# Kernel optimization log

Measured on AMD Instinct MI355X. Metric: run time of the kernel, lower is better.

Reference implementation:

```python
import jax, jax.numpy as jnp
import numpy as np

IN_FEATURES = 100000
OUT_FEATURES = 256

def setup_inputs() -> dict:
    key = jax.random.key(0)
    k1, k2 = jax.random.split(key)
    size = IN_FEATURES
    # adj: COO indices [2, nnz] with nnz == size (values are all ones in the module)
    adj = jax.random.randint(k1, (2, size), 0, size, dtype=jnp.int64)
    weight = jax.random.normal(k2, (IN_FEATURES, OUT_FEATURES), dtype=jnp.float32) * (1.0 / np.sqrt(IN_FEATURES))
    return {"adj": adj, "size": size, "weight": weight}

def reference(adj, size, weight):
    # sparse (size, size) COO with values=1 at (adj[0], adj[1]), times dense weight:
    # out[r] = sum over edges (r, c) of 1.0 * weight[c]
    rows = adj[0]
    cols = adj[1]
    gathered = weight[cols]  # [nnz, out_features] gather
    out = jax.ops.segment_sum(gathered, rows, num_segments=size)  # [size, out_features]
    return out
```

## Files before the change

### kernel.cpp

```cpp
#include <hip/hip_runtime.h>


constexpr int OUT_F = 256;
constexpr int CAP = 8;
constexpr int MAXOVF = 16384;

using f32x4 = __attribute__((ext_vector_type(4))) float;
using i32x4 = __attribute__((ext_vector_type(4))) int;


__global__ __launch_bounds__(256) void fill_k(const int* __restrict__ rows,
                                              const int* __restrict__ cols,
                                              int* __restrict__ counts,
                                              int* __restrict__ bucket,
                                              int* __restrict__ ovf_n,
                                              int* __restrict__ ovf,
                                              int nnz) {
    int e = blockIdx.x * 256 + threadIdx.x;
    if (e >= nnz) return;
    int r = rows[e];
    int c = cols[e];
    int slot = atomicAdd(&counts[r], 1);
    if (slot < CAP) {
        bucket[r * CAP + slot] = c;
    } else {
        int o = atomicAdd(ovf_n, 1);
        if (o < MAXOVF) { ovf[2 * o] = r; ovf[2 * o + 1] = c; }
    }
}


__device__ __forceinline__ void ovf_scan(f32x4& acc, int row,
                                         const int* __restrict__ ovf_n,
                                         const int* __restrict__ ovf,
                                         const f32x4* __restrict__ w4, int lane) {
    int m = *ovf_n; if (m > MAXOVF) m = MAXOVF;
    for (int j = 0; j < m; j++) {
        if (ovf[2 * j] == row)
            acc += w4[(size_t)ovf[2 * j + 1] * 64 + lane];
    }
}

__device__ __forceinline__ void rare_tail(f32x4& acc, int n, const i32x4& b0,
                                          const i32x4* __restrict__ bucket4, int row,
                                          const f32x4* __restrict__ w4, int lane,
                                          const int* __restrict__ ovf_n,
                                          const int* __restrict__ ovf) {
    int m = n < CAP ? n : CAP;
    acc += w4[(size_t)__builtin_amdgcn_readfirstlane(b0.z) * 64 + lane];
    if (m > 3) acc += w4[(size_t)__builtin_amdgcn_readfirstlane(b0.w) * 64 + lane];
    if (m > 4) {
        i32x4 b1 = __builtin_nontemporal_load(bucket4 + (size_t)row * 2 + 1);
        acc += w4[(size_t)__builtin_amdgcn_readfirstlane(b1.x) * 64 + lane];
        if (m > 5) acc += w4[(size_t)__builtin_amdgcn_readfirstlane(b1.y) * 64 + lane];
        if (m > 6) acc += w4[(size_t)__builtin_amdgcn_readfirstlane(b1.z) * 64 + lane];
        if (m > 7) acc += w4[(size_t)__builtin_amdgcn_readfirstlane(b1.w) * 64 + lane];
        if (n > CAP) ovf_scan(acc, row, ovf_n, ovf, w4, lane);
    }
}

__global__ __launch_bounds__(256) void gather_k(const int* __restrict__ counts,
                                                const i32x4* __restrict__ bucket4,
                                                const f32x4* __restrict__ w4,
                                                f32x4* __restrict__ out4,
                                                const int* __restrict__ ovf_n,
                                                const int* __restrict__ ovf,
                                                int nrows) {
    const int lane = threadIdx.x & 63;
    int wid = (blockIdx.x << 2) + (threadIdx.x >> 6);
    wid = __builtin_amdgcn_readfirstlane(wid);
    const int row0 = wid << 2;
    if (row0 >= nrows) return;

    const f32x4 z = {0.f, 0.f, 0.f, 0.f};

    if (row0 + 4 <= nrows) {
        const i32x4 cntv = __builtin_nontemporal_load((const i32x4*)(counts + row0));
        const int n0 = __builtin_amdgcn_readfirstlane(cntv.x);
        const int n1 = __builtin_amdgcn_readfirstlane(cntv.y);
        const int n2 = __builtin_amdgcn_readfirstlane(cntv.z);
        const int n3 = __builtin_amdgcn_readfirstlane(cntv.w);

        f32x4* o = out4 + (size_t)row0 * 64 + lane;
        if ((n0 | n1 | n2 | n3) == 0) {
            __builtin_nontemporal_store(z, o);
            __builtin_nontemporal_store(z, o + 64);
            __builtin_nontemporal_store(z, o + 128);
            __builtin_nontemporal_store(z, o + 192);
            return;
        }

        i32x4 ba, bb, bc, bd;
        if (n0 > 0) ba = __builtin_nontemporal_load(bucket4 + (size_t)(row0 + 0) * 2);
        if (n1 > 0) bb = __builtin_nontemporal_load(bucket4 + (size_t)(row0 + 1) * 2);
        if (n2 > 0) bc = __builtin_nontemporal_load(bucket4 + (size_t)(row0 + 2) * 2);
        if (n3 > 0) bd = __builtin_nontemporal_load(bucket4 + (size_t)(row0 + 3) * 2);

        f32x4 va0, va1, vb0, vb1, vc0, vc1, vd0, vd1;
        if (n0 > 0) va0 = w4[(size_t)__builtin_amdgcn_readfirstlane(ba.x) * 64 + lane];
        if (n0 > 1) va1 = w4[(size_t)__builtin_amdgcn_readfirstlane(ba.y) * 64 + lane];
        if (n1 > 0) vb0 = w4[(size_t)__builtin_amdgcn_readfirstlane(bb.x) * 64 + lane];
        if (n1 > 1) vb1 = w4[(size_t)__builtin_amdgcn_readfirstlane(bb.y) * 64 + lane];
        if (n2 > 0) vc0 = w4[(size_t)__builtin_amdgcn_readfirstlane(bc.x) * 64 + lane];
        if (n2 > 1) vc1 = w4[(size_t)__builtin_amdgcn_readfirstlane(bc.y) * 64 + lane];
        if (n3 > 0) vd0 = w4[(size_t)__builtin_amdgcn_readfirstlane(bd.x) * 64 + lane];
        if (n3 > 1) vd1 = w4[(size_t)__builtin_amdgcn_readfirstlane(bd.y) * 64 + lane];

        f32x4 a0 = z, a1 = z, a2 = z, a3 = z;
        if (n0 > 0) {
            a0 = va0;
            if (n0 > 1) a0 += va1;
            if (n0 > 2) rare_tail(a0, n0, ba, bucket4, row0 + 0, w4, lane, ovf_n, ovf);
        }
        if (n1 > 0) {
            a1 = vb0;
            if (n1 > 1) a1 += vb1;
            if (n1 > 2) rare_tail(a1, n1, bb, bucket4, row0 + 1, w4, lane, ovf_n, ovf);
        }
        if (n2 > 0) {
            a2 = vc0;
            if (n2 > 1) a2 += vc1;
            if (n2 > 2) rare_tail(a2, n2, bc, bucket4, row0 + 2, w4, lane, ovf_n, ovf);
        }
        if (n3 > 0) {
            a3 = vd0;
            if (n3 > 1) a3 += vd1;
            if (n3 > 2) rare_tail(a3, n3, bd, bucket4, row0 + 3, w4, lane, ovf_n, ovf);
        }

        __builtin_nontemporal_store(a0, o);
        __builtin_nontemporal_store(a1, o + 64);
        __builtin_nontemporal_store(a2, o + 128);
        __builtin_nontemporal_store(a3, o + 192);
    } else {
        for (int r = row0; r < nrows; r++) {
            const int n = counts[r];
            f32x4 acc = z;
            if (n > 0) {
                const i32x4 b0 = bucket4[(size_t)r * 2];
                acc += w4[(size_t)__builtin_amdgcn_readfirstlane(b0.x) * 64 + lane];
                if (n > 1) acc += w4[(size_t)__builtin_amdgcn_readfirstlane(b0.y) * 64 + lane];
                if (n > 2) rare_tail(acc, n, b0, bucket4, r, w4, lane, ovf_n, ovf);
            }
            __builtin_nontemporal_store(acc, out4 + (size_t)r * 64 + lane);
        }
    }
}


__global__ __launch_bounds__(256) void zero_f4(float4* __restrict__ out, int n4) {
    int i = blockIdx.x * 256 + threadIdx.x;
    if (i < n4) out[i] = make_float4(0.f, 0.f, 0.f, 0.f);
}

__global__ __launch_bounds__(256) void scatter_kernel(const int* __restrict__ rows,
                                                      const int* __restrict__ cols,
                                                      const float* __restrict__ weight,
                                                      float* __restrict__ out, int nnz) {
    const int lane = threadIdx.x & 63;
    const int edge = blockIdx.x * 4 + (threadIdx.x >> 6);
    if (edge >= nnz) return;
    const int r = rows[edge];
    const int c = cols[edge];
    const float4 v = ((const float4*)(weight + (size_t)c * OUT_F))[lane];
    float* o = out + (size_t)r * OUT_F + (size_t)lane * 4;
    atomicAdd(o + 0, v.x);
    atomicAdd(o + 1, v.y);
    atomicAdd(o + 2, v.z);
    atomicAdd(o + 3, v.w);
}


extern "C" void kernel_launch(void* const* d_in, const int* in_sizes, int n_in,
                              void* d_out, int out_size, void* d_ws, size_t ws_size,
                              hipStream_t stream) {
    const int* adj = (const int*)d_in[0];
    const int nnz = in_sizes[0] / 2;
    const int* rows = adj;
    const int* cols = adj + nnz;
    const float* weight = (const float*)d_in[2];
    float* out = (float*)d_out;
    const int nrows = out_size / OUT_F;

    const size_t ovfnOff   = (size_t)nrows;
    const size_t ovfOff    = ovfnOff + 4;
    const size_t bucketOff = ovfOff + 2 * MAXOVF;
    const size_t need      = (bucketOff + (size_t)nrows * CAP) * 4;

    if (ws_size >= need && (nrows & 3) == 0) {
        int* wsI    = (int*)d_ws;
        int* counts = wsI;
        int* ovf_n  = wsI + ovfnOff;
        int* ovf    = wsI + ovfOff;
        int* bucket = wsI + bucketOff;

        hipMemsetAsync(counts, 0, ovfOff * 4, stream);
        fill_k<<<(nnz + 255) / 256, 256, 0, stream>>>(rows, cols, counts, bucket,
                                                      ovf_n, ovf, nnz);
        gather_k<<<(nrows + 15) / 16, 256, 0, stream>>>(counts, (const i32x4*)bucket,
                                                        (const f32x4*)weight,
                                                        (f32x4*)out, ovf_n, ovf, nrows);
    } else {
        const int n4 = out_size / 4;
        zero_f4<<<(n4 + 255) / 256, 256, 0, stream>>>((float4*)out, n4);
        scatter_kernel<<<(nnz + 3) / 4, 256, 0, stream>>>(rows, cols, weight, out, nnz);
    }
}
```

Before: 195.1 us.

## Fuse memset, bucket fill and gather into one cooperative kernel with grid syncs

Replaces the memset plus two kernel launches with a single cooperative kernel that zeroes counts, fills row buckets with atomics, then gathers and sums weight rows. Grid-wide syncs separate the phases and the gather phase uses a grid-stride loop over row quads, prefetching the next counts vector. This removes launch overheads and inter-kernel gaps. In exchange it adds grid sync costs and limits the grid to the co-resident occupancy, and it falls back to the old path if the cooperative launch fails.

```diff
diff --git a/kernel.cpp b/kernel.cpp
--- a/kernel.cpp
+++ b/kernel.cpp
@@ -1,4 +1,7 @@
 #include <hip/hip_runtime.h>
+#include <hip/hip_cooperative_groups.h>
+
+namespace cg = cooperative_groups;
 
 
 constexpr int OUT_F = 256;
@@ -7,6 +10,157 @@
 
 using f32x4 = __attribute__((ext_vector_type(4))) float;
 using i32x4 = __attribute__((ext_vector_type(4))) int;
+
+
+__device__ __forceinline__ void ovf_scan(f32x4& acc, int row,
+                                         const int* __restrict__ ovf_n,
+                                         const int* __restrict__ ovf,
+                                         const f32x4* __restrict__ w4, int lane) {
+    int m = *ovf_n; if (m > MAXOVF) m = MAXOVF;
+    for (int j = 0; j < m; j++) {
+        if (ovf[2 * j] == row)
+            acc += w4[(size_t)ovf[2 * j + 1] * 64 + lane];
+    }
+}
+
+__device__ __forceinline__ void rare_tail(f32x4& acc, int n, const i32x4& b0,
+                                          const i32x4* __restrict__ bucket4, int row,
+                                          const f32x4* __restrict__ w4, int lane,
+                                          const int* __restrict__ ovf_n,
+                                          const int* __restrict__ ovf) {
+    int m = n < CAP ? n : CAP;
+    acc += w4[(size_t)__builtin_amdgcn_readfirstlane(b0.z) * 64 + lane];
+    if (m > 3) acc += w4[(size_t)__builtin_amdgcn_readfirstlane(b0.w) * 64 + lane];
+    if (m > 4) {
+        i32x4 b1 = __builtin_nontemporal_load(bucket4 + (size_t)row * 2 + 1);
+        acc += w4[(size_t)__builtin_amdgcn_readfirstlane(b1.x) * 64 + lane];
+        if (m > 5) acc += w4[(size_t)__builtin_amdgcn_readfirstlane(b1.y) * 64 + lane];
+        if (m > 6) acc += w4[(size_t)__builtin_amdgcn_readfirstlane(b1.z) * 64 + lane];
+        if (m > 7) acc += w4[(size_t)__builtin_amdgcn_readfirstlane(b1.w) * 64 + lane];
+        if (n > CAP) ovf_scan(acc, row, ovf_n, ovf, w4, lane);
+    }
+}
+
+__device__ __forceinline__ void process_quad(int row0, const i32x4& cntv,
+                                             const i32x4* __restrict__ bucket4,
+                                             const f32x4* __restrict__ w4,
+                                             f32x4* __restrict__ out4,
+                                             const int* __restrict__ ovf_n,
+                                             const int* __restrict__ ovf, int lane) {
+    const f32x4 z = {0.f, 0.f, 0.f, 0.f};
+    const int n0 = __builtin_amdgcn_readfirstlane(cntv.x);
+    const int n1 = __builtin_amdgcn_readfirstlane(cntv.y);
+    const int n2 = __builtin_amdgcn_readfirstlane(cntv.z);
+    const int n3 = __builtin_amdgcn_readfirstlane(cntv.w);
+
+    f32x4* o = out4 + (size_t)row0 * 64 + lane;
+    if ((n0 | n1 | n2 | n3) == 0) {
+        __builtin_nontemporal_store(z, o);
+        __builtin_nontemporal_store(z, o + 64);
+        __builtin_nontemporal_store(z, o + 128);
+        __builtin_nontemporal_store(z, o + 192);
+        return;
+    }
+
+    i32x4 ba, bb, bc, bd;
+    if (n0 > 0) ba = __builtin_nontemporal_load(bucket4 + (size_t)(row0 + 0) * 2);
+    if (n1 > 0) bb = __builtin_nontemporal_load(bucket4 + (size_t)(row0 + 1) * 2);
+    if (n2 > 0) bc = __builtin_nontemporal_load(bucket4 + (size_t)(row0 + 2) * 2);
+    if (n3 > 0) bd = __builtin_nontemporal_load(bucket4 + (size_t)(row0 + 3) * 2);
+
+    f32x4 va0, va1, vb0, vb1, vc0, vc1, vd0, vd1;
+    if (n0 > 0) va0 = w4[(size_t)__builtin_amdgcn_readfirstlane(ba.x) * 64 + lane];
+    if (n0 > 1) va1 = w4[(size_t)__builtin_amdgcn_readfirstlane(ba.y) * 64 + lane];
+    if (n1 > 0) vb0 = w4[(size_t)__builtin_amdgcn_readfirstlane(bb.x) * 64 + lane];
+    if (n1 > 1) vb1 = w4[(size_t)__builtin_amdgcn_readfirstlane(bb.y) * 64 + lane];
+    if (n2 > 0) vc0 = w4[(size_t)__builtin_amdgcn_readfirstlane(bc.x) * 64 + lane];
+    if (n2 > 1) vc1 = w4[(size_t)__builtin_amdgcn_readfirstlane(bc.y) * 64 + lane];
+    if (n3 > 0) vd0 = w4[(size_t)__builtin_amdgcn_readfirstlane(bd.x) * 64 + lane];
+    if (n3 > 1) vd1 = w4[(size_t)__builtin_amdgcn_readfirstlane(bd.y) * 64 + lane];
+
+    f32x4 a0 = z, a1 = z, a2 = z, a3 = z;
+    if (n0 > 0) {
+        a0 = va0;
+        if (n0 > 1) a0 += va1;
+        if (n0 > 2) rare_tail(a0, n0, ba, bucket4, row0 + 0, w4, lane, ovf_n, ovf);
+    }
+    if (n1 > 0) {
+        a1 = vb0;
+        if (n1 > 1) a1 += vb1;
+        if (n1 > 2) rare_tail(a1, n1, bb, bucket4, row0 + 1, w4, lane, ovf_n, ovf);
+    }
+    if (n2 > 0) {
+        a2 = vc0;
+        if (n2 > 1) a2 += vc1;
+        if (n2 > 2) rare_tail(a2, n2, bc, bucket4, row0 + 2, w4, lane, ovf_n, ovf);
+    }
+    if (n3 > 0) {
+        a3 = vd0;
+        if (n3 > 1) a3 += vd1;
+        if (n3 > 2) rare_tail(a3, n3, bd, bucket4, row0 + 3, w4, lane, ovf_n, ovf);
+    }
+
+    __builtin_nontemporal_store(a0, o);
+    __builtin_nontemporal_store(a1, o + 64);
+    __builtin_nontemporal_store(a2, o + 128);
+    __builtin_nontemporal_store(a3, o + 192);
+}
+
+
+__global__ __launch_bounds__(256) void fused_k(const int* __restrict__ rows,
+                                               const int* __restrict__ cols,
+                                               int* __restrict__ counts,
+                                               int* __restrict__ bucket,
+                                               int* __restrict__ ovf_n,
+                                               int* __restrict__ ovf,
+                                               const f32x4* __restrict__ w4,
+                                               f32x4* __restrict__ out4,
+                                               int nnz, int nrows) {
+    cg::grid_group grid = cg::this_grid();
+    const int tid = blockIdx.x * 256 + threadIdx.x;
+    const int nthreads = gridDim.x * 256;
+
+    for (int i = tid; i < nrows + 4; i += nthreads) counts[i] = 0;
+
+    __threadfence();
+    grid.sync();
+
+    for (int e = tid; e < nnz; e += nthreads) {
+        int r = __builtin_nontemporal_load(rows + e);
+        int c = __builtin_nontemporal_load(cols + e);
+        int slot = atomicAdd(&counts[r], 1);
+        if (slot < CAP) {
+            bucket[r * CAP + slot] = c;
+        } else {
+            int o = atomicAdd(ovf_n, 1);
+            if (o < MAXOVF) { ovf[2 * o] = r; ovf[2 * o + 1] = c; }
+        }
+    }
+
+    __threadfence();
+    grid.sync();
+
+    const int lane = threadIdx.x & 63;
+    int wid = (blockIdx.x << 2) + (threadIdx.x >> 6);
+    wid = __builtin_amdgcn_readfirstlane(wid);
+    const int nwaves = gridDim.x << 2;
+    const int nquads = nrows >> 2;
+    const i32x4* bucket4 = (const i32x4*)bucket;
+
+    int q = wid;
+    if (q >= nquads) return;
+    i32x4 cntv = __builtin_nontemporal_load((const i32x4*)(counts + (q << 2)));
+    while (true) {
+        const int qn = q + nwaves;
+        i32x4 cnext;
+        if (qn < nquads)
+            cnext = __builtin_nontemporal_load((const i32x4*)(counts + (qn << 2)));
+        process_quad(q << 2, cntv, bucket4, w4, out4, ovf_n, ovf, lane);
+        if (qn >= nquads) break;
+        cntv = cnext;
+        q = qn;
+    }
+}
 
 
 __global__ __launch_bounds__(256) void fill_k(const int* __restrict__ rows,
@@ -29,36 +183,6 @@
     }
 }
 
-
-__device__ __forceinline__ void ovf_scan(f32x4& acc, int row,
-                                         const int* __restrict__ ovf_n,
-                                         const int* __restrict__ ovf,
-                                         const f32x4* __restrict__ w4, int lane) {
-    int m = *ovf_n; if (m > MAXOVF) m = MAXOVF;
-    for (int j = 0; j < m; j++) {
-        if (ovf[2 * j] == row)
-            acc += w4[(size_t)ovf[2 * j + 1] * 64 + lane];
-    }
-}
-
-__device__ __forceinline__ void rare_tail(f32x4& acc, int n, const i32x4& b0,
-                                          const i32x4* __restrict__ bucket4, int row,
-                                          const f32x4* __restrict__ w4, int lane,
-                                          const int* __restrict__ ovf_n,
-                                          const int* __restrict__ ovf) {
-    int m = n < CAP ? n : CAP;
-    acc += w4[(size_t)__builtin_amdgcn_readfirstlane(b0.z) * 64 + lane];
-    if (m > 3) acc += w4[(size_t)__builtin_amdgcn_readfirstlane(b0.w) * 64 + lane];
-    if (m > 4) {
-        i32x4 b1 = __builtin_nontemporal_load(bucket4 + (size_t)row * 2 + 1);
-        acc += w4[(size_t)__builtin_amdgcn_readfirstlane(b1.x) * 64 + lane];
-        if (m > 5) acc += w4[(size_t)__builtin_amdgcn_readfirstlane(b1.y) * 64 + lane];
-        if (m > 6) acc += w4[(size_t)__builtin_amdgcn_readfirstlane(b1.z) * 64 + lane];
-        if (m > 7) acc += w4[(size_t)__builtin_amdgcn_readfirstlane(b1.w) * 64 + lane];
-        if (n > CAP) ovf_scan(acc, row, ovf_n, ovf, w4, lane);
-    }
-}
-
 __global__ __launch_bounds__(256) void gather_k(const int* __restrict__ counts,
                                                 const i32x4* __restrict__ bucket4,
                                                 const f32x4* __restrict__ w4,
@@ -72,67 +196,11 @@
     const int row0 = wid << 2;
     if (row0 >= nrows) return;
 
-    const f32x4 z = {0.f, 0.f, 0.f, 0.f};
-
     if (row0 + 4 <= nrows) {
         const i32x4 cntv = __builtin_nontemporal_load((const i32x4*)(counts + row0));
-        const int n0 = __builtin_amdgcn_readfirstlane(cntv.x);
-        const int n1 = __builtin_amdgcn_readfirstlane(cntv.y);
-        const int n2 = __builtin_amdgcn_readfirstlane(cntv.z);
-        const int n3 = __builtin_amdgcn_readfirstlane(cntv.w);
-
-        f32x4* o = out4 + (size_t)row0 * 64 + lane;
-        if ((n0 | n1 | n2 | n3) == 0) {
-            __builtin_nontemporal_store(z, o);
-            __builtin_nontemporal_store(z, o + 64);
-            __builtin_nontemporal_store(z, o + 128);
-            __builtin_nontemporal_store(z, o + 192);
-            return;
-        }
-
-        i32x4 ba, bb, bc, bd;
-        if (n0 > 0) ba = __builtin_nontemporal_load(bucket4 + (size_t)(row0 + 0) * 2);
-        if (n1 > 0) bb = __builtin_nontemporal_load(bucket4 + (size_t)(row0 + 1) * 2);
-        if (n2 > 0) bc = __builtin_nontemporal_load(bucket4 + (size_t)(row0 + 2) * 2);
-        if (n3 > 0) bd = __builtin_nontemporal_load(bucket4 + (size_t)(row0 + 3) * 2);
-
-        f32x4 va0, va1, vb0, vb1, vc0, vc1, vd0, vd1;
-        if (n0 > 0) va0 = w4[(size_t)__builtin_amdgcn_readfirstlane(ba.x) * 64 + lane];
-        if (n0 > 1) va1 = w4[(size_t)__builtin_amdgcn_readfirstlane(ba.y) * 64 + lane];
-        if (n1 > 0) vb0 = w4[(size_t)__builtin_amdgcn_readfirstlane(bb.x) * 64 + lane];
-        if (n1 > 1) vb1 = w4[(size_t)__builtin_amdgcn_readfirstlane(bb.y) * 64 + lane];
-        if (n2 > 0) vc0 = w4[(size_t)__builtin_amdgcn_readfirstlane(bc.x) * 64 + lane];
-        if (n2 > 1) vc1 = w4[(size_t)__builtin_amdgcn_readfirstlane(bc.y) * 64 + lane];
-        if (n3 > 0) vd0 = w4[(size_t)__builtin_amdgcn_readfirstlane(bd.x) * 64 + lane];
-        if (n3 > 1) vd1 = w4[(size_t)__builtin_amdgcn_readfirstlane(bd.y) * 64 + lane];
-
-        f32x4 a0 = z, a1 = z, a2 = z, a3 = z;
-        if (n0 > 0) {
-            a0 = va0;
-            if (n0 > 1) a0 += va1;
-            if (n0 > 2) rare_tail(a0, n0, ba, bucket4, row0 + 0, w4, lane, ovf_n, ovf);
-        }
-        if (n1 > 0) {
-            a1 = vb0;
-            if (n1 > 1) a1 += vb1;
-            if (n1 > 2) rare_tail(a1, n1, bb, bucket4, row0 + 1, w4, lane, ovf_n, ovf);
-        }
-        if (n2 > 0) {
-            a2 = vc0;
-            if (n2 > 1) a2 += vc1;
-            if (n2 > 2) rare_tail(a2, n2, bc, bucket4, row0 + 2, w4, lane, ovf_n, ovf);
-        }
-        if (n3 > 0) {
-            a3 = vd0;
-            if (n3 > 1) a3 += vd1;
-            if (n3 > 2) rare_tail(a3, n3, bd, bucket4, row0 + 3, w4, lane, ovf_n, ovf);
-        }
-
-        __builtin_nontemporal_store(a0, o);
-        __builtin_nontemporal_store(a1, o + 64);
-        __builtin_nontemporal_store(a2, o + 128);
-        __builtin_nontemporal_store(a3, o + 192);
+        process_quad(row0, cntv, bucket4, w4, out4, ovf_n, ovf, lane);
     } else {
+        const f32x4 z = {0.f, 0.f, 0.f, 0.f};
         for (int r = row0; r < nrows; r++) {
             const int n = counts[r];
             f32x4 acc = z;
@@ -194,6 +262,34 @@
         int* ovf    = wsI + ovfOff;
         int* bucket = wsI + bucketOff;
 
+        static int coopGrid = 0;
+        if (coopGrid == 0) {
+            int perCU = 0;
+            if (hipOccupancyMaxActiveBlocksPerMultiprocessor(
+                    &perCU, (const void*)fused_k, 256, 0) != hipSuccess || perCU <= 0)
+                perCU = 2;
+            int nCU = 256;
+            hipDeviceProp_t prop;
+            if (hipGetDeviceProperties(&prop, 0) == hipSuccess &&
+                prop.multiProcessorCount > 0)
+                nCU = prop.multiProcessorCount;
+            coopGrid = perCU * nCU;
+        }
+        int needBlocks = (nrows / 4 + 3) / 4;
+        int nb1 = (nnz + 255) / 256;
+        if (nb1 > needBlocks) needBlocks = nb1;
+        int grid = coopGrid < needBlocks ? coopGrid : needBlocks;
+        if (grid < 1) grid = 1;
+
+        const f32x4* w4v  = (const f32x4*)weight;
+        f32x4*       o4v  = (f32x4*)out;
+        void* kargs[] = {(void*)&rows, (void*)&cols, (void*)&counts, (void*)&bucket,
+                         (void*)&ovf_n, (void*)&ovf, (void*)&w4v, (void*)&o4v,
+                         (void*)&nnz, (void*)&nrows};
+        hipError_t e = hipLaunchCooperativeKernel((const void*)fused_k, dim3(grid),
+                                                  dim3(256), kargs, 0, stream);
+        if (e == hipSuccess) return;
+
         hipMemsetAsync(counts, 0, ovfOff * 4, stream);
         fill_k<<<(nnz + 255) / 256, 256, 0, stream>>>(rows, cols, counts, bucket,
                                                       ovf_n, ovf, nnz);
```

Measured after the change: 494.0 us. 153% more time.
